# Kernel optimization log

Hardware: AMD Instinct MI355X
Metric: run time of the kernel (lower is better)

## Reference

```python
import jax, jax.numpy as jnp
import numpy as np

N_IN, N_HID, N_OUT = 200_000, 600_000, 200_000
N = N_IN + N_HID + N_OUT
E = 16_000_000


def setup_inputs() -> dict:
    key = jax.random.key(0)
    k1, k2, k3, k4, k5, k6, k7, k8 = jax.random.split(key, 8)
    x_input = jax.random.normal(k1, (N_IN, 1), dtype=jnp.float32)
    edge_index = jax.random.randint(k2, (2, E), 0, N, dtype=jnp.int64)
    edge_attr = jax.random.normal(k3, (E,), dtype=jnp.float32)
    # deterministic node layout: first N_IN are type 0, then type 1, then type 2
    node_types = jnp.concatenate([
        jnp.zeros((N_IN,), jnp.int64),
        jnp.ones((N_HID,), jnp.int64),
        jnp.full((N_OUT,), 2, jnp.int64),
    ])
    bias_vec = jax.random.normal(k4, (N,), dtype=jnp.float32)
    # Linear(1,1) params for the two MLPForwardLayers
    w1 = jax.random.normal(k5, (1, 1), dtype=jnp.float32)
    b1 = jax.random.normal(k6, (1,), dtype=jnp.float32)
    w2 = jax.random.normal(k7, (1, 1), dtype=jnp.float32)
    b2 = jax.random.normal(k8, (1,), dtype=jnp.float32)
    return {"x_input": x_input, "edge_attr": edge_attr, "bias_vec": bias_vec,
            "w1": w1, "b1": b1, "w2": w2, "b2": b2,
            "edge_index": edge_index, "node_types": node_types, "n_out": N_OUT}


def reference(x_input, edge_attr, bias_vec, w1, b1, w2, b2, edge_index, node_types, n_out):
    n = bias_vec.shape[0]
    bias = bias_vec[:, None]                      # [N,1]
    src, dst = edge_index[0], edge_index[1]       # [E]
    t_src = node_types[src]
    t_dst = node_types[dst]

    # x starts as zeros; input nodes (type 0, laid out first) get x_input
    x = jnp.zeros_like(bias).at[: x_input.shape[0]].set(x_input)  # [N,1]

    # layer 1: edges from type-0 -> type-1, gather * weight, scatter-add
    m1 = ((t_src == 0) & (t_dst == 1)).astype(edge_attr.dtype)
    msg1 = x[src, 0] * edge_attr * m1             # [E]
    agg1 = jax.ops.segment_sum(msg1, dst, num_segments=n)[:, None]
    h = jax.nn.relu((agg1 + bias) @ w1.T + b1)    # Linear(1,1) + ReLU
    x = jnp.where((node_types == 1)[:, None], h, x)

    # layer 2: edges from type-1 -> type-2
    m2 = ((t_src == 1) & (t_dst == 2)).astype(edge_attr.dtype)
    msg2 = x[src, 0] * edge_attr * m2
    agg2 = jax.ops.segment_sum(msg2, dst, num_segments=n)[:, None]
    out = (agg2 + bias) @ w2.T + b2               # no activation

    # output nodes (type 2) are the last n_out nodes
    return out[n - n_out:]
```

## Files before the change

kernel.cpp:

```cpp
#include <hip/hip_runtime.h>

#define N_IN_C   200000
#define N_HID_C  600000
#define N_OUT_C  200000
#define E_C      16000000
#define HID_BASE 200000
#define OUT_BASE 800000

#define R1_SHIFT 14
#define R1_SIZE  (1 << R1_SHIFT)
#define NB1      37
#define R2_SHIFT 12
#define R2_SIZE  (1 << R2_SHIFT)
#define NB2      49
#define NBU      (NB1 + NB2)
#define OVF2_CAP 65536
#define BIN_T    256
#define EPT      8

template<int DO1, int DO2>
__global__ __launch_bounds__(BIN_T) void phase_bin(
    const int* __restrict__ src, const int* __restrict__ dst,
    const float* __restrict__ attr, const float* __restrict__ x_input,
    int2* __restrict__ seg1, int* __restrict__ cnt1_g, int cap1,
    int2* __restrict__ seg2, int* __restrict__ cnt2_g, int cap2,
    float* __restrict__ ovf1,
    int4* __restrict__ ovf2, unsigned int* __restrict__ ovf2_cur,
    unsigned long long* __restrict__ trash)
{
    __shared__ int cntU[NBU + 1];
    for (int u = threadIdx.x; u < NBU + 1; u += BIN_T) cntU[u] = 0;
    __syncthreads();

    int2* __restrict__ my1 = seg1 + (size_t)blockIdx.x * NB1 * cap1;
    int2* __restrict__ my2 = seg2 + (size_t)blockIdx.x * NB2 * cap2;

    const long long tid  = (long long)blockIdx.x * BIN_T + threadIdx.x;
    unsigned long long* __restrict__ my_trash = trash + tid;
    const long long step = (long long)gridDim.x * BIN_T * EPT;

    long long base = tid * EPT;
    bool valid = base < (long long)E_C;
    long long pb = valid ? base : 0;
    int4   csA = *reinterpret_cast<const int4*>(src + pb);
    int4   csB = *reinterpret_cast<const int4*>(src + pb + 4);
    int4   cdA = *reinterpret_cast<const int4*>(dst + pb);
    int4   cdB = *reinterpret_cast<const int4*>(dst + pb + 4);
    float4 caA = *reinterpret_cast<const float4*>(attr + pb);
    float4 caB = *reinterpret_cast<const float4*>(attr + pb + 4);

    while (valid) {
        const long long nbase  = base + step;
        const bool      nvalid = nbase < (long long)E_C;
        const long long npb    = nvalid ? nbase : 0;
        const int4   nsA = *reinterpret_cast<const int4*>(src + npb);
        const int4   nsB = *reinterpret_cast<const int4*>(src + npb + 4);
        const int4   ndA = *reinterpret_cast<const int4*>(dst + npb);
        const int4   ndB = *reinterpret_cast<const int4*>(dst + npb + 4);
        const float4 naA = *reinterpret_cast<const float4*>(attr + npb);
        const float4 naB = *reinterpret_cast<const float4*>(attr + npb + 4);

        const int   sE[EPT] = {csA.x, csA.y, csA.z, csA.w, csB.x, csB.y, csB.z, csB.w};
        const int   dE[EPT] = {cdA.x, cdA.y, cdA.z, cdA.w, cdB.x, cdB.y, cdB.z, cdB.w};
        const float aE[EPT] = {caA.x, caA.y, caA.z, caA.w, caB.x, caB.y, caB.z, caB.w};

        #pragma unroll
        for (int k = 0; k < EPT; ++k) {
            const int s_ = sE[k], d_ = dE[k];
            const float a_ = aE[k];
            const bool is1 = DO1 && ((unsigned)s_ < (unsigned)N_IN_C) &&
                             ((unsigned)(d_ - HID_BASE) < (unsigned)N_HID_C);
            const bool is2 = DO2 && ((unsigned)(s_ - HID_BASE) < (unsigned)N_HID_C) &&
                             (d_ >= OUT_BASE);
            const int dl = is1 ? (d_ - HID_BASE) : (d_ - OUT_BASE);
            const int ul = is1 ? (dl >> R1_SHIFT)
                               : (is2 ? (NB1 + (dl >> R2_SHIFT)) : NBU);
            const int slot = atomicAdd(&cntU[ul], 1);

            const unsigned key = is1
                ? (((unsigned)s_ << R1_SHIFT) | (unsigned)(dl & (R1_SIZE - 1)))
                : (((unsigned)(s_ - HID_BASE) << R2_SHIFT) |
                   (unsigned)(dl & (R2_SIZE - 1)));
            const unsigned long long rec =
                ((unsigned long long)(unsigned)__float_as_int(a_) << 32) | key;
            const bool real1 = is1 && (slot < cap1);
            const bool real2 = is2 && (slot < cap2);
            unsigned long long* addr =
                real1 ? reinterpret_cast<unsigned long long*>(my1 + ul * cap1 + slot)
              : real2 ? reinterpret_cast<unsigned long long*>(my2 + (ul - NB1) * cap2 + slot)
              :         my_trash;
            *addr = rec;

            if (is1 && slot >= cap1)
                atomicAdd(&ovf1[dl], x_input[s_] * a_);
            if (is2 && slot >= cap2) {
                const unsigned p = atomicAdd(ovf2_cur, 1u);
                if (p < OVF2_CAP)
                    ovf2[p] = make_int4(s_ - HID_BASE, dl, __float_as_int(a_), 0);
            }
        }

        csA = nsA; csB = nsB; cdA = ndA; cdB = ndB; caA = naA; caB = naB;
        base = nbase; valid = nvalid;
    }

    __syncthreads();
    if (DO1 && threadIdx.x < NB1)
        cnt1_g[blockIdx.x * NB1 + threadIdx.x] = cntU[threadIdx.x];
    if (DO2 && threadIdx.x >= NB1 && threadIdx.x < NBU)
        cnt2_g[blockIdx.x * NB2 + (threadIdx.x - NB1)] = cntU[threadIdx.x];
}

template<int CAP1>
__global__ __launch_bounds__(1024) void reduce1(
    const int2* __restrict__ seg1, const int* __restrict__ cnt1_g,
    int npb, const float* __restrict__ x_input, float* __restrict__ partial1)
{
    __shared__ float table[R1_SIZE];
    for (int j = threadIdx.x; j < R1_SIZE; j += 1024) table[j] = 0.f;
    __syncthreads();

    const int b    = blockIdx.x;
    const int sbeg = blockIdx.y * npb;
    const int tot  = npb * CAP1;
    for (int t = threadIdx.x; t < tot; t += 1024) {
        const int bl  = t / CAP1;
        const int i   = t - bl * CAP1;
        const int blk = sbeg + bl;
        if (i < min(cnt1_g[blk * NB1 + b], CAP1)) {
            const int2 r = seg1[((size_t)blk * NB1 + b) * CAP1 + i];
            const unsigned sx = (unsigned)r.x >> R1_SHIFT;
            atomicAdd(&table[r.x & (R1_SIZE - 1)],
                      x_input[sx] * __int_as_float(r.y));
        }
    }
    __syncthreads();

    float* dstp = partial1 + ((size_t)blockIdx.y * NB1 + b) * R1_SIZE;
    for (int j = threadIdx.x; j < R1_SIZE; j += 1024) dstp[j] = table[j];
}

__global__ __launch_bounds__(256) void final1(
    const float* __restrict__ partial1, int S1,
    const float* __restrict__ ovf1, const float* __restrict__ bias_vec,
    const float* __restrict__ w1p, const float* __restrict__ b1p,
    float* __restrict__ h)
{
    const int i = blockIdx.x * 256 + threadIdx.x;
    if (i >= N_HID_C) return;
    const int b = i >> R1_SHIFT, j = i & (R1_SIZE - 1);
    float acc = ovf1[i];
    for (int s = 0; s < S1; ++s)
        acc += partial1[((size_t)s * NB1 + b) * R1_SIZE + j];
    float v = fmaf(acc + bias_vec[HID_BASE + i], w1p[0], b1p[0]);
    h[i] = v > 0.f ? v : 0.f;
}

template<int CAP2>
__global__ __launch_bounds__(1024) void reduce2(
    const int2* __restrict__ seg2, const int* __restrict__ cnt2_g,
    int npb, const float* __restrict__ h,
    const int4* __restrict__ ovf2, const unsigned int* __restrict__ ovf2_cur,
    float* __restrict__ partial2)
{
    __shared__ float table[R2_SIZE];
    for (int j = threadIdx.x; j < R2_SIZE; j += 1024) table[j] = 0.f;
    __syncthreads();

    const int b    = blockIdx.x;
    const int sbeg = blockIdx.y * npb;
    const int tot  = npb * CAP2;
    for (int t = threadIdx.x; t < tot; t += 1024) {
        const int bl  = t / CAP2;
        const int i   = t - bl * CAP2;
        const int blk = sbeg + bl;
        if (i < min(cnt2_g[blk * NB2 + b], CAP2)) {
            const int2 r = seg2[((size_t)blk * NB2 + b) * CAP2 + i];
            const int sl = (int)((unsigned)r.x >> R2_SHIFT);
            atomicAdd(&table[r.x & (R2_SIZE - 1)], h[sl] * __int_as_float(r.y));
        }
    }
    if (blockIdx.y == 0) {
        const unsigned no = min(*ovf2_cur, (unsigned)OVF2_CAP);
        for (unsigned i = threadIdx.x; i < no; i += 1024) {
            const int4 r = ovf2[i];
            if ((r.y >> R2_SHIFT) == b)
                atomicAdd(&table[r.y & (R2_SIZE - 1)], h[r.x] * __int_as_float(r.z));
        }
    }
    __syncthreads();

    float* dstp = partial2 + ((size_t)blockIdx.y * NB2 + b) * R2_SIZE;
    for (int j = threadIdx.x; j < R2_SIZE; j += 1024) dstp[j] = table[j];
}

__global__ __launch_bounds__(256) void final2(
    const float* __restrict__ partial2, int S2,
    const float* __restrict__ bias_vec,
    const float* __restrict__ w2p, const float* __restrict__ b2p,
    float* __restrict__ out)
{
    const int i = blockIdx.x * 256 + threadIdx.x;
    if (i >= N_OUT_C) return;
    const int b = i >> R2_SHIFT, j = i & (R2_SIZE - 1);
    float acc = 0.f;
    for (int s = 0; s < S2; ++s)
        acc += partial2[((size_t)s * NB2 + b) * R2_SIZE + j];
    out[i] = fmaf(acc + bias_vec[OUT_BASE + i], w2p[0], b2p[0]);
}

__global__ __launch_bounds__(256) void fb_pass1(
    const int* __restrict__ src, const int* __restrict__ dst,
    const float* __restrict__ attr, const float* __restrict__ x_input,
    float* __restrict__ agg1)
{
    const long long tid    = (long long)blockIdx.x * 256 + threadIdx.x;
    const long long stride = (long long)gridDim.x * 256;
    for (long long base = tid * 4; base < (long long)E_C; base += stride * 4) {
        const int4   s4 = *reinterpret_cast<const int4*>(src + base);
        const int4   d4 = *reinterpret_cast<const int4*>(dst + base);
        const float4 a4 = *reinterpret_cast<const float4*>(attr + base);
        int s, d;
        s = s4.x; d = d4.x;
        if ((unsigned)s < (unsigned)N_IN_C && (unsigned)(d - HID_BASE) < (unsigned)N_HID_C)
            atomicAdd(&agg1[d - HID_BASE], x_input[s] * a4.x);
        s = s4.y; d = d4.y;
        if ((unsigned)s < (unsigned)N_IN_C && (unsigned)(d - HID_BASE) < (unsigned)N_HID_C)
            atomicAdd(&agg1[d - HID_BASE], x_input[s] * a4.y);
        s = s4.z; d = d4.z;
        if ((unsigned)s < (unsigned)N_IN_C && (unsigned)(d - HID_BASE) < (unsigned)N_HID_C)
            atomicAdd(&agg1[d - HID_BASE], x_input[s] * a4.z);
        s = s4.w; d = d4.w;
        if ((unsigned)s < (unsigned)N_IN_C && (unsigned)(d - HID_BASE) < (unsigned)N_HID_C)
            atomicAdd(&agg1[d - HID_BASE], x_input[s] * a4.w);
    }
}

__global__ __launch_bounds__(256) void fb_hid(
    float* __restrict__ agg1, const float* __restrict__ bias_vec,
    const float* __restrict__ w1, const float* __restrict__ b1)
{
    const int i = blockIdx.x * 256 + threadIdx.x;
    if (i < N_HID_C) {
        float v = fmaf(agg1[i] + bias_vec[HID_BASE + i], w1[0], b1[0]);
        agg1[i] = v > 0.0f ? v : 0.0f;
    }
}

__global__ __launch_bounds__(256) void fb_pass2(
    const int* __restrict__ src, const int* __restrict__ dst,
    const float* __restrict__ attr, const float* __restrict__ h,
    float* __restrict__ out)
{
    const long long tid    = (long long)blockIdx.x * 256 + threadIdx.x;
    const long long stride = (long long)gridDim.x * 256;
    for (long long base = tid * 4; base < (long long)E_C; base += stride * 4) {
        const int4   s4 = *reinterpret_cast<const int4*>(src + base);
        const int4   d4 = *reinterpret_cast<const int4*>(dst + base);
        const float4 a4 = *reinterpret_cast<const float4*>(attr + base);
        int s, d;
        s = s4.x; d = d4.x;
        if ((unsigned)(s - HID_BASE) < (unsigned)N_HID_C && d >= OUT_BASE)
            atomicAdd(&out[d - OUT_BASE], h[s - HID_BASE] * a4.x);
        s = s4.y; d = d4.y;
        if ((unsigned)(s - HID_BASE) < (unsigned)N_HID_C && d >= OUT_BASE)
            atomicAdd(&out[d - OUT_BASE], h[s - HID_BASE] * a4.y);
        s = s4.z; d = d4.z;
        if ((unsigned)(s - HID_BASE) < (unsigned)N_HID_C && d >= OUT_BASE)
            atomicAdd(&out[d - OUT_BASE], h[s - HID_BASE] * a4.z);
        s = s4.w; d = d4.w;
        if ((unsigned)(s - HID_BASE) < (unsigned)N_HID_C && d >= OUT_BASE)
            atomicAdd(&out[d - OUT_BASE], h[s - HID_BASE] * a4.w);
    }
}

__global__ __launch_bounds__(256) void fb_out(
    float* __restrict__ out, const float* __restrict__ bias_vec,
    const float* __restrict__ w2, const float* __restrict__ b2)
{
    const int i = blockIdx.x * 256 + threadIdx.x;
    if (i < N_OUT_C)
        out[i] = fmaf(out[i] + bias_vec[OUT_BASE + i], w2[0], b2[0]);
}

extern "C" void kernel_launch(void* const* d_in, const int* in_sizes, int n_in,
                              void* d_out, int out_size, void* d_ws, size_t ws_size,
                              hipStream_t stream) {
    const float* x_input   = (const float*)d_in[0];
    const float* edge_attr = (const float*)d_in[1];
    const float* bias_vec  = (const float*)d_in[2];
    const float* w1        = (const float*)d_in[3];
    const float* b1        = (const float*)d_in[4];
    const float* w2        = (const float*)d_in[5];
    const float* b2        = (const float*)d_in[6];
    const int*   edge_idx  = (const int*)d_in[7];

    const int* src = edge_idx;
    const int* dst = edge_idx + E_C;
    float* out = (float*)d_out;

    const int cfg_nblk[4] = {1024, 512, 256, 128};
    const int cfg_cap1[4] = {  96, 160, 288, 544};
    const int cfg_cap2[4] = {  80, 128, 232, 424};

    const size_t P1_B = (size_t)NB1 * R1_SIZE * 4;
    const size_t P2_B = (size_t)NB2 * R2_SIZE * 4;
    const size_t TRASH_B = (size_t)1024 * BIN_T * 8;
    const size_t fixed_b = 2400128  + 2400128
                         + (size_t)OVF2_CAP * 16 + TRASH_B + 512;

    int mode = 2, ci = -1, S1 = 1, S2 = 1;
    for (int m = 0; m < 2 && mode == 2; ++m) {
        for (int c = 0; c < 4 && mode == 2; ++c) {
            const size_t nblk = cfg_nblk[c];
            const size_t cnt_b  = nblk * (NB1 + NB2) * 4 + 256;
            const size_t seg1_b = nblk * NB1 * (size_t)cfg_cap1[c] * 8;
            const size_t seg2_b = nblk * NB2 * (size_t)cfg_cap2[c] * 8;
            const size_t seg_b  = (m == 0) ? (seg1_b + seg2_b)
                                           : (seg1_b > seg2_b ? seg1_b : seg2_b);
            const size_t base   = fixed_b + cnt_b + seg_b + 1024;
            if (base + P1_B + P2_B > ws_size) continue;
            mode = m; ci = c;
            size_t rem = ws_size - base;
            for (int s = 8; s >= 1; s >>= 1)
                if ((size_t)s * P1_B + P2_B <= rem) { S1 = s; break; }
            rem -= (size_t)S1 * P1_B;
            for (int s = 8; s >= 1; s >>= 1)
                if ((size_t)s * P2_B <= rem) { S2 = s; break; }
        }
    }

    if (mode == 2) {
        float* agg1 = (float*)d_ws;
        (void)hipMemsetAsync(agg1, 0, (size_t)N_HID_C * sizeof(float), stream);
        (void)hipMemsetAsync(out,  0, (size_t)N_OUT_C * sizeof(float), stream);
        fb_pass1<<<2048, 256, 0, stream>>>(src, dst, edge_attr, x_input, agg1);
        fb_hid<<<(N_HID_C + 255) / 256, 256, 0, stream>>>(agg1, bias_vec, w1, b1);
        fb_pass2<<<2048, 256, 0, stream>>>(src, dst, edge_attr, agg1, out);
        fb_out<<<(N_OUT_C + 255) / 256, 256, 0, stream>>>(out, bias_vec, w2, b2);
        return;
    }

    const int nblk = cfg_nblk[ci];
    const int cap1 = cfg_cap1[ci];
    const int cap2 = cfg_cap2[ci];
    const int npb1 = nblk / S1;
    const int npb2 = nblk / S2;

    char* w = (char*)d_ws;
    size_t off = 0;
    auto take = [&](size_t bytes) {
        off = (off + 127) & ~(size_t)127;
        char* p = w + off; off += bytes; return p;
    };
    float*              ovf1     = (float*)take((size_t)N_HID_C * 4);
    float*              h        = (float*)take((size_t)N_HID_C * 4);
    int4*               ovf2     = (int4*)take((size_t)OVF2_CAP * 16);
    unsigned int*       ovf2_cur = (unsigned int*)take(128);
    unsigned long long* trash    = (unsigned long long*)take(TRASH_B);
    int*                cnt1_g   = (int*)take((size_t)nblk * NB1 * 4);
    int*                cnt2_g   = (int*)take((size_t)nblk * NB2 * 4);
    float*              partial1 = (float*)take((size_t)S1 * P1_B);
    float*              partial2 = (float*)take((size_t)S2 * P2_B);
    int2 *seg1, *seg2;
    if (mode == 0) {
        seg1 = (int2*)take((size_t)nblk * NB1 * (size_t)cap1 * 8);
        seg2 = (int2*)take((size_t)nblk * NB2 * (size_t)cap2 * 8);
    } else {
        const size_t s1 = (size_t)nblk * NB1 * (size_t)cap1 * 8;
        const size_t s2 = (size_t)nblk * NB2 * (size_t)cap2 * 8;
        char* shared = take(s1 > s2 ? s1 : s2);
        seg1 = (int2*)shared;
        seg2 = (int2*)shared;
    }

    (void)hipMemsetAsync(ovf1, 0, (size_t)N_HID_C * sizeof(float), stream);
    (void)hipMemsetAsync(ovf2_cur, 0, sizeof(unsigned int), stream);

    if (mode == 0) {
        phase_bin<1, 1><<<nblk, BIN_T, 0, stream>>>(
            src, dst, edge_attr, x_input,
            seg1, cnt1_g, cap1, seg2, cnt2_g, cap2, ovf1, ovf2, ovf2_cur, trash);
    } else {
        phase_bin<1, 0><<<nblk, BIN_T, 0, stream>>>(
            src, dst, edge_attr, x_input,
            seg1, cnt1_g, cap1, seg2, cnt2_g, cap2, ovf1, ovf2, ovf2_cur, trash);
    }

    dim3 g1(NB1, S1);
    switch (ci) {
    case 0: reduce1< 96><<<g1, 1024, 0, stream>>>(seg1, cnt1_g, npb1, x_input, partial1); break;
    case 1: reduce1<160><<<g1, 1024, 0, stream>>>(seg1, cnt1_g, npb1, x_input, partial1); break;
    case 2: reduce1<288><<<g1, 1024, 0, stream>>>(seg1, cnt1_g, npb1, x_input, partial1); break;
    default: reduce1<544><<<g1, 1024, 0, stream>>>(seg1, cnt1_g, npb1, x_input, partial1); break;
    }
    final1<<<(N_HID_C + 255) / 256, 256, 0, stream>>>(
        partial1, S1, ovf1, bias_vec, w1, b1, h);

    if (mode == 1) {
        phase_bin<0, 1><<<nblk, BIN_T, 0, stream>>>(
            src, dst, edge_attr, x_input,
            seg1, cnt1_g, cap1, seg2, cnt2_g, cap2, ovf1, ovf2, ovf2_cur, trash);
    }

    dim3 g2(NB2, S2);
    switch (ci) {
    case 0: reduce2< 80><<<g2, 1024, 0, stream>>>(seg2, cnt2_g, npb2, h, ovf2, ovf2_cur, partial2); break;
    case 1: reduce2<128><<<g2, 1024, 0, stream>>>(seg2, cnt2_g, npb2, h, ovf2, ovf2_cur, partial2); break;
    case 2: reduce2<232><<<g2, 1024, 0, stream>>>(seg2, cnt2_g, npb2, h, ovf2, ovf2_cur, partial2); break;
    default: reduce2<424><<<g2, 1024, 0, stream>>>(seg2, cnt2_g, npb2, h, ovf2, ovf2_cur, partial2); break;
    }
    final2<<<(N_OUT_C + 255) / 256, 256, 0, stream>>>(
        partial2, S2, bias_vec, w2, b2, out);
}
```

Measured before the change: 139.1 us.

## Stage binned edge records in per-wave LDS rings and flush 64-byte chunks

The binning kernel now writes each classified edge record into a per-wave shared-memory ring for its bucket. Whenever eight records accumulate, it flushes them to the global segment as four int4 stores instead of one scattered 8-byte store per edge. Irrelevant edges no longer go to a trash buffer, and leftover partial rings are flushed with padding at the end. Block counts and capacities are retuned to match. The risks are padded records with zero weight, more LDS use and atomic contention, and a concurrency hazard: a wave may overwrite a ring half while another lane is still reading it for a flush.

New measurement: 128.8 us. 1.08x faster.

```diff
diff --git a/kernel.cpp b/kernel.cpp
--- a/kernel.cpp
+++ b/kernel.cpp
@@ -16,6 +16,8 @@
 #define NBU      (NB1 + NB2)
 #define OVF2_CAP 65536
 #define BIN_T    256
+#define WAVES    (BIN_T / 64)
+#define RING_D   16
 #define EPT      8
 
 template<int DO1, int DO2>
@@ -25,18 +27,22 @@
     int2* __restrict__ seg1, int* __restrict__ cnt1_g, int cap1,
     int2* __restrict__ seg2, int* __restrict__ cnt2_g, int cap2,
     float* __restrict__ ovf1,
-    int4* __restrict__ ovf2, unsigned int* __restrict__ ovf2_cur,
-    unsigned long long* __restrict__ trash)
-{
-    __shared__ int cntU[NBU + 1];
-    for (int u = threadIdx.x; u < NBU + 1; u += BIN_T) cntU[u] = 0;
-    __syncthreads();
+    int4* __restrict__ ovf2, unsigned int* __restrict__ ovf2_cur)
+{
+    __shared__ __align__(64) int2 ring[WAVES][NBU][RING_D];
+    __shared__ int wcnt[WAVES][NBU];
+    __shared__ int lcnt[NBU];
+    for (int i = threadIdx.x; i < WAVES * NBU; i += BIN_T) (&wcnt[0][0])[i] = 0;
+    for (int i = threadIdx.x; i < NBU; i += BIN_T) lcnt[i] = 0;
+    __syncthreads();
+
+    const int w    = threadIdx.x >> 6;
+    const int lane = threadIdx.x & 63;
 
     int2* __restrict__ my1 = seg1 + (size_t)blockIdx.x * NB1 * cap1;
     int2* __restrict__ my2 = seg2 + (size_t)blockIdx.x * NB2 * cap2;
 
     const long long tid  = (long long)blockIdx.x * BIN_T + threadIdx.x;
-    unsigned long long* __restrict__ my_trash = trash + tid;
     const long long step = (long long)gridDim.x * BIN_T * EPT;
 
     long long base = tid * EPT;
@@ -72,31 +78,50 @@
                              ((unsigned)(d_ - HID_BASE) < (unsigned)N_HID_C);
             const bool is2 = DO2 && ((unsigned)(s_ - HID_BASE) < (unsigned)N_HID_C) &&
                              (d_ >= OUT_BASE);
-            const int dl = is1 ? (d_ - HID_BASE) : (d_ - OUT_BASE);
-            const int ul = is1 ? (dl >> R1_SHIFT)
-                               : (is2 ? (NB1 + (dl >> R2_SHIFT)) : NBU);
-            const int slot = atomicAdd(&cntU[ul], 1);
-
-            const unsigned key = is1
-                ? (((unsigned)s_ << R1_SHIFT) | (unsigned)(dl & (R1_SIZE - 1)))
-                : (((unsigned)(s_ - HID_BASE) << R2_SHIFT) |
-                   (unsigned)(dl & (R2_SIZE - 1)));
-            const unsigned long long rec =
-                ((unsigned long long)(unsigned)__float_as_int(a_) << 32) | key;
-            const bool real1 = is1 && (slot < cap1);
-            const bool real2 = is2 && (slot < cap2);
-            unsigned long long* addr =
-                real1 ? reinterpret_cast<unsigned long long*>(my1 + ul * cap1 + slot)
-              : real2 ? reinterpret_cast<unsigned long long*>(my2 + (ul - NB1) * cap2 + slot)
-              :         my_trash;
-            *addr = rec;
-
-            if (is1 && slot >= cap1)
-                atomicAdd(&ovf1[dl], x_input[s_] * a_);
-            if (is2 && slot >= cap2) {
-                const unsigned p = atomicAdd(ovf2_cur, 1u);
-                if (p < OVF2_CAP)
-                    ovf2[p] = make_int4(s_ - HID_BASE, dl, __float_as_int(a_), 0);
+            if (is1 || is2) {
+                const int dl = is1 ? (d_ - HID_BASE) : (d_ - OUT_BASE);
+                const int u  = is1 ? (dl >> R1_SHIFT) : (NB1 + (dl >> R2_SHIFT));
+                const unsigned key = is1
+                    ? (((unsigned)s_ << R1_SHIFT) | (unsigned)(dl & (R1_SIZE - 1)))
+                    : (((unsigned)(s_ - HID_BASE) << R2_SHIFT) |
+                       (unsigned)(dl & (R2_SIZE - 1)));
+                const int slot = atomicAdd(&wcnt[w][u], 1);
+                ring[w][u][slot & (RING_D - 1)] = make_int2((int)key, __float_as_int(a_));
+                if ((slot & 7) == 7) {
+                    const int half = (slot >> 3) & 1;
+                    const int cap  = (u < NB1) ? cap1 : cap2;
+                    const int L    = atomicAdd(&lcnt[u], 1);
+                    const int4* rp = reinterpret_cast<const int4*>(&ring[w][u][half * 8]);
+                    const int4 q0 = rp[0], q1 = rp[1], q2 = rp[2], q3 = rp[3];
+                    if (L * 8 + 8 <= cap) {
+                        int4* p = (u < NB1)
+                            ? reinterpret_cast<int4*>(my1 + (size_t)u * cap1 + L * 8)
+                            : reinterpret_cast<int4*>(my2 + (size_t)(u - NB1) * cap2 + L * 8);
+                        p[0] = q0; p[1] = q1; p[2] = q2; p[3] = q3;
+                    } else {
+                        const int2 rr[8] = {
+                            make_int2(q0.x, q0.y), make_int2(q0.z, q0.w),
+                            make_int2(q1.x, q1.y), make_int2(q1.z, q1.w),
+                            make_int2(q2.x, q2.y), make_int2(q2.z, q2.w),
+                            make_int2(q3.x, q3.y), make_int2(q3.z, q3.w)};
+                        #pragma unroll
+                        for (int j = 0; j < 8; ++j) {
+                            const unsigned kk = (unsigned)rr[j].x;
+                            const float aa = __int_as_float(rr[j].y);
+                            if (u < NB1) {
+                                const int node = (u << R1_SHIFT) | (int)(kk & (R1_SIZE - 1));
+                                atomicAdd(&ovf1[node], x_input[kk >> R1_SHIFT] * aa);
+                            } else {
+                                const unsigned p2 = atomicAdd(ovf2_cur, 1u);
+                                if (p2 < OVF2_CAP)
+                                    ovf2[p2] = make_int4(
+                                        (int)(kk >> R2_SHIFT),
+                                        ((u - NB1) << R2_SHIFT) | (int)(kk & (R2_SIZE - 1)),
+                                        rr[j].y, 0);
+                            }
+                        }
+                    }
+                }
             }
         }
 
@@ -105,10 +130,51 @@
     }
 
     __syncthreads();
+    for (int u = lane; u < NBU; u += 64) {
+        const int c = wcnt[w][u];
+        const int r = c & 7;
+        if (r) {
+            const int half = (c >> 3) & 1;
+            const int cap  = (u < NB1) ? cap1 : cap2;
+            const int L    = atomicAdd(&lcnt[u], 1);
+            int2 rec[8];
+            #pragma unroll
+            for (int j = 0; j < 8; ++j)
+                rec[j] = (j < r) ? ring[w][u][half * 8 + j] : make_int2(j, 0);
+            if (L * 8 + 8 <= cap) {
+                int4* p = (u < NB1)
+                    ? reinterpret_cast<int4*>(my1 + (size_t)u * cap1 + L * 8)
+                    : reinterpret_cast<int4*>(my2 + (size_t)(u - NB1) * cap2 + L * 8);
+                p[0] = make_int4(rec[0].x, rec[0].y, rec[1].x, rec[1].y);
+                p[1] = make_int4(rec[2].x, rec[2].y, rec[3].x, rec[3].y);
+                p[2] = make_int4(rec[4].x, rec[4].y, rec[5].x, rec[5].y);
+                p[3] = make_int4(rec[6].x, rec[6].y, rec[7].x, rec[7].y);
+            } else {
+                for (int j = 0; j < r; ++j) {
+                    const unsigned kk = (unsigned)rec[j].x;
+                    const float aa = __int_as_float(rec[j].y);
+                    if (u < NB1) {
+                        const int node = (u << R1_SHIFT) | (int)(kk & (R1_SIZE - 1));
+                        atomicAdd(&ovf1[node], x_input[kk >> R1_SHIFT] * aa);
+                    } else {
+                        const unsigned p2 = atomicAdd(ovf2_cur, 1u);
+                        if (p2 < OVF2_CAP)
+                            ovf2[p2] = make_int4(
+                                (int)(kk >> R2_SHIFT),
+                                ((u - NB1) << R2_SHIFT) | (int)(kk & (R2_SIZE - 1)),
+                                rec[j].y, 0);
+                    }
+                }
+            }
+        }
+    }
+    __syncthreads();
+
     if (DO1 && threadIdx.x < NB1)
-        cnt1_g[blockIdx.x * NB1 + threadIdx.x] = cntU[threadIdx.x];
+        cnt1_g[blockIdx.x * NB1 + threadIdx.x] = min(lcnt[threadIdx.x] * 8, cap1);
     if (DO2 && threadIdx.x >= NB1 && threadIdx.x < NBU)
-        cnt2_g[blockIdx.x * NB2 + (threadIdx.x - NB1)] = cntU[threadIdx.x];
+        cnt2_g[blockIdx.x * NB2 + (threadIdx.x - NB1)] =
+            min(lcnt[threadIdx.x] * 8, cap2);
 }
 
 template<int CAP1>
@@ -299,15 +365,14 @@
     const int* dst = edge_idx + E_C;
     float* out = (float*)d_out;
 
-    const int cfg_nblk[4] = {1024, 512, 256, 128};
-    const int cfg_cap1[4] = {  96, 160, 288, 544};
-    const int cfg_cap2[4] = {  80, 128, 232, 424};
+    const int cfg_nblk[4] = { 768, 512, 384, 256};
+    const int cfg_cap1[4] = { 152, 200, 248, 336};
+    const int cfg_cap2[4] = { 128, 168, 200, 272};
 
     const size_t P1_B = (size_t)NB1 * R1_SIZE * 4;
     const size_t P2_B = (size_t)NB2 * R2_SIZE * 4;
-    const size_t TRASH_B = (size_t)1024 * BIN_T * 8;
     const size_t fixed_b = 2400128  + 2400128
-                         + (size_t)OVF2_CAP * 16 + TRASH_B + 512;
+                         + (size_t)OVF2_CAP * 16 + 512;
 
     int mode = 2, ci = -1, S1 = 1, S2 = 1;
     for (int m = 0; m < 2 && mode == 2; ++m) {
@@ -353,15 +418,14 @@
         off = (off + 127) & ~(size_t)127;
         char* p = w + off; off += bytes; return p;
     };
-    float*              ovf1     = (float*)take((size_t)N_HID_C * 4);
-    float*              h        = (float*)take((size_t)N_HID_C * 4);
-    int4*               ovf2     = (int4*)take((size_t)OVF2_CAP * 16);
-    unsigned int*       ovf2_cur = (unsigned int*)take(128);
-    unsigned long long* trash    = (unsigned long long*)take(TRASH_B);
-    int*                cnt1_g   = (int*)take((size_t)nblk * NB1 * 4);
-    int*                cnt2_g   = (int*)take((size_t)nblk * NB2 * 4);
-    float*              partial1 = (float*)take((size_t)S1 * P1_B);
-    float*              partial2 = (float*)take((size_t)S2 * P2_B);
+    float*        ovf1     = (float*)take((size_t)N_HID_C * 4);
+    float*        h        = (float*)take((size_t)N_HID_C * 4);
+    int4*         ovf2     = (int4*)take((size_t)OVF2_CAP * 16);
+    unsigned int* ovf2_cur = (unsigned int*)take(128);
+    int*          cnt1_g   = (int*)take((size_t)nblk * NB1 * 4);
+    int*          cnt2_g   = (int*)take((size_t)nblk * NB2 * 4);
+    float*        partial1 = (float*)take((size_t)S1 * P1_B);
+    float*        partial2 = (float*)take((size_t)S2 * P2_B);
     int2 *seg1, *seg2;
     if (mode == 0) {
         seg1 = (int2*)take((size_t)nblk * NB1 * (size_t)cap1 * 8);
@@ -380,19 +444,19 @@
     if (mode == 0) {
         phase_bin<1, 1><<<nblk, BIN_T, 0, stream>>>(
             src, dst, edge_attr, x_input,
-            seg1, cnt1_g, cap1, seg2, cnt2_g, cap2, ovf1, ovf2, ovf2_cur, trash);
+            seg1, cnt1_g, cap1, seg2, cnt2_g, cap2, ovf1, ovf2, ovf2_cur);
     } else {
         phase_bin<1, 0><<<nblk, BIN_T, 0, stream>>>(
             src, dst, edge_attr, x_input,
-            seg1, cnt1_g, cap1, seg2, cnt2_g, cap2, ovf1, ovf2, ovf2_cur, trash);
+            seg1, cnt1_g, cap1, seg2, cnt2_g, cap2, ovf1, ovf2, ovf2_cur);
     }
 
     dim3 g1(NB1, S1);
     switch (ci) {
-    case 0: reduce1< 96><<<g1, 1024, 0, stream>>>(seg1, cnt1_g, npb1, x_input, partial1); break;
-    case 1: reduce1<160><<<g1, 1024, 0, stream>>>(seg1, cnt1_g, npb1, x_input, partial1); break;
-    case 2: reduce1<288><<<g1, 1024, 0, stream>>>(seg1, cnt1_g, npb1, x_input, partial1); break;
-    default: reduce1<544><<<g1, 1024, 0, stream>>>(seg1, cnt1_g, npb1, x_input, partial1); break;
+    case 0: reduce1<152><<<g1, 1024, 0, stream>>>(seg1, cnt1_g, npb1, x_input, partial1); break;
+    case 1: reduce1<200><<<g1, 1024, 0, stream>>>(seg1, cnt1_g, npb1, x_input, partial1); break;
+    case 2: reduce1<248><<<g1, 1024, 0, stream>>>(seg1, cnt1_g, npb1, x_input, partial1); break;
+    default: reduce1<336><<<g1, 1024, 0, stream>>>(seg1, cnt1_g, npb1, x_input, partial1); break;
     }
     final1<<<(N_HID_C + 255) / 256, 256, 0, stream>>>(
         partial1, S1, ovf1, bias_vec, w1, b1, h);
@@ -400,15 +464,15 @@
     if (mode == 1) {
         phase_bin<0, 1><<<nblk, BIN_T, 0, stream>>>(
             src, dst, edge_attr, x_input,
-            seg1, cnt1_g, cap1, seg2, cnt2_g, cap2, ovf1, ovf2, ovf2_cur, trash);
+            seg1, cnt1_g, cap1, seg2, cnt2_g, cap2, ovf1, ovf2, ovf2_cur);
     }
 
     dim3 g2(NB2, S2);
     switch (ci) {
-    case 0: reduce2< 80><<<g2, 1024, 0, stream>>>(seg2, cnt2_g, npb2, h, ovf2, ovf2_cur, partial2); break;
-    case 1: reduce2<128><<<g2, 1024, 0, stream>>>(seg2, cnt2_g, npb2, h, ovf2, ovf2_cur, partial2); break;
-    case 2: reduce2<232><<<g2, 1024, 0, stream>>>(seg2, cnt2_g, npb2, h, ovf2, ovf2_cur, partial2); break;
-    default: reduce2<424><<<g2, 1024, 0, stream>>>(seg2, cnt2_g, npb2, h, ovf2, ovf2_cur, partial2); break;
+    case 0: reduce2<128><<<g2, 1024, 0, stream>>>(seg2, cnt2_g, npb2, h, ovf2, ovf2_cur, partial2); break;
+    case 1: reduce2<168><<<g2, 1024, 0, stream>>>(seg2, cnt2_g, npb2, h, ovf2, ovf2_cur, partial2); break;
+    case 2: reduce2<200><<<g2, 1024, 0, stream>>>(seg2, cnt2_g, npb2, h, ovf2, ovf2_cur, partial2); break;
+    default: reduce2<272><<<g2, 1024, 0, stream>>>(seg2, cnt2_g, npb2, h, ovf2, ovf2_cur, partial2); break;
     }
     final2<<<(N_OUT_C + 255) / 256, 256, 0, stream>>>(
         partial2, S2, bias_vec, w2, b2, out);
```
